# Performance work log

Measured on AMD Instinct MI355X. Metric: run time of the kernel, lower is better.

## Reference

```python
import jax, jax.numpy as jnp
import numpy as np

B, N, D, H = 64, 196, 768, 3072
QMAX = 127.0  # 8-bit symmetric: clamp to [-128, 127]


def ste_round(x):
    # straight-through-estimator round (QAT)
    return x + jax.lax.stop_gradient(jnp.round(x) - x)


def q_linear_diag(x, w, b, a_sf):
    """Quantized diagonal linear (ResMLP Affine / LayerScale as QuantLinear)."""
    w_sf = jnp.max(jnp.abs(w)) / QMAX            # per-tensor weight scale
    w_int = ste_round(w / w_sf)                  # int8 weights (|.|<=127)
    out_int = (x / a_sf) * w_int
    if b is not None:
        out_int = out_int + ste_round(b / (a_sf * w_sf))  # 32-bit bias
    return out_int * (a_sf * w_sf), w_sf


def q_linear_dense(x, w, b, a_sf):
    """Quantized dense linear: int8 GEMM + int32 bias, dequant with a_sf*w_sf."""
    w_sf = jnp.max(jnp.abs(w)) / QMAX
    w_int = jnp.clip(ste_round(w / w_sf), -QMAX - 1, QMAX)
    out_int = jnp.einsum('...i,oi->...o', x / a_sf, w_int) + ste_round(b / (a_sf * w_sf))
    return out_int * (a_sf * w_sf), w_sf


def q_act(x, pre_sf, new_sf, identity=None, id_sf=None):
    """HAWQ-style QuantAct: fixed-point requantization to scale new_sf (8-bit)."""
    if identity is None:
        z_int = ste_round(x / pre_sf)
        out_int = ste_round(z_int * (pre_sf / new_sf))
    else:
        # main branch (x - identity) requantized with pre_sf, identity with id_sf
        z_int = ste_round((x - identity) / pre_sf)
        out_int = ste_round(z_int * (pre_sf / new_sf)) \
                + ste_round(ste_round(identity / id_sf) * (id_sf / new_sf))
    out_int = jnp.clip(out_int, -QMAX - 1, QMAX)
    return out_int * new_sf, new_sf


def _forward(x, norm1_w, norm1_b, attn_w, attn_b, gamma1_w,
             norm2_w, norm2_b, fc1_w, fc1_b, fc2_w, fc2_b, gamma2_w, act_sfs):
    a_sf = act_sfs[0]
    # --- token-mixing half ---
    identity, id_sf = x, a_sf
    x, w_sf = q_linear_diag(x, norm1_w, norm1_b, a_sf)         # norm1 (affine)
    x = jnp.swapaxes(x, 1, 2)                                  # [B, D, N]
    x, a_sf = q_act(x, a_sf * w_sf, act_sfs[1])                # quant_act1
    x, w_sf = q_linear_dense(x, attn_w, attn_b, a_sf)          # attn (cross-patch)
    x = jnp.swapaxes(x, 1, 2)                                  # [B, N, D]
    x, a_sf = q_act(x, a_sf * w_sf, act_sfs[2])                # quant_act2
    x, w_sf = q_linear_diag(x, gamma1_w, None, a_sf)           # gamma_1 (layerscale)
    x = x + identity
    x, a_sf = q_act(x, a_sf * w_sf, act_sfs[3], identity, id_sf)  # quant_act_int32_1
    # --- MLP half ---
    identity, id_sf = x, a_sf
    x, w_sf = q_linear_diag(x, norm2_w, norm2_b, a_sf)         # norm2
    x, a_sf = q_act(x, a_sf * w_sf, act_sfs[4])                # quant_act3
    x, w_sf = q_linear_dense(x, fc1_w, fc1_b, a_sf)            # mlp.fc1
    x = jax.nn.relu(x)
    x, a_sf = q_act(x, a_sf * w_sf, act_sfs[5])                # mlp.quant_act1
    x, w_sf = q_linear_dense(x, fc2_w, fc2_b, a_sf)            # mlp.fc2
    x, a_sf = q_act(x, a_sf * w_sf, act_sfs[6])                # mlp.quant_act2
    x, w_sf = q_linear_diag(x, gamma2_w, None, a_sf)           # gamma_2
    x = x + identity
    x, a_sf = q_act(x, a_sf * w_sf, act_sfs[7], identity, id_sf)  # quant_act_int32_2
    return x, a_sf


def setup_inputs() -> dict:
    key = jax.random.key(0)
    ks = jax.random.split(key, 16)
    act_sfs = jax.random.uniform(ks[14], (8,), jnp.float32, 0.02, 0.06)
    x = jax.random.normal(ks[0], (B, N, D), jnp.float32)
    # input is already quantized at scale act_sfs[0]
    x = jnp.clip(jnp.round(x / act_sfs[0]), -128, 127) * act_sfs[0]
    s = 0.05
    return {
        'x': x,
        'norm1_w': 1.0 + s * jax.random.normal(ks[1], (D,), jnp.float32),
        'norm1_b': s * jax.random.normal(ks[2], (D,), jnp.float32),
        'attn_w': jax.random.normal(ks[3], (N, N), jnp.float32) / np.sqrt(N),
        'attn_b': s * jax.random.normal(ks[4], (N,), jnp.float32),
        'gamma1_w': 0.1 + s * jax.random.normal(ks[5], (D,), jnp.float32),
        'norm2_w': 1.0 + s * jax.random.normal(ks[6], (D,), jnp.float32),
        'norm2_b': s * jax.random.normal(ks[7], (D,), jnp.float32),
        'fc1_w': jax.random.normal(ks[8], (H, D), jnp.float32) / np.sqrt(D),
        'fc1_b': s * jax.random.normal(ks[9], (H,), jnp.float32),
        'fc2_w': jax.random.normal(ks[10], (D, H), jnp.float32) / np.sqrt(H),
        'fc2_b': s * jax.random.normal(ks[11], (D,), jnp.float32),
        'gamma2_w': 0.1 + s * jax.random.normal(ks[12], (D,), jnp.float32),
        'act_sfs': act_sfs,
    }


def reference(x, norm1_w, norm1_b, attn_w, attn_b, gamma1_w,
              norm2_w, norm2_b, fc1_w, fc1_b, fc2_w, fc2_b, gamma2_w, act_sfs):
    return _forward(x, norm1_w, norm1_b, attn_w, attn_b, gamma1_w,
                    norm2_w, norm2_b, fc1_w, fc1_b, fc2_w, fc2_b, gamma2_w, act_sfs)
```

## Files before the change

### kernel.cpp

```cpp
#include <hip/hip_runtime.h>

#define B_ 64
#define N_ 196
#define D_ 768
#define H_ 3072
#define M_ (B_*N_)
#define NP 256

typedef int int4v __attribute__((ext_vector_type(4)));
typedef signed char i8;

#define WS_MAX 0
#define WS_W1F 16
#define WS_B1F (16+768)
#define WS_G1F (16+768*2)
#define WS_W2F (16+768*3)
#define WS_B2F (16+768*4)
#define WS_G2F (16+768*5)
#define WS_BA  (16+768*6)
#define WS_BF1 (WS_BA+256)
#define WS_BF2 (WS_BF1+3072)
#define OFF_WA   40960ull
#define OFF_FC1  (OFF_WA+65536ull)
#define OFF_FC2  (OFF_FC1+2359296ull)
#define OFF_X2   (OFF_FC2+2359296ull)
#define OFF_Q3   (OFF_X2+9633792ull)
#define OFF_Q4   (OFF_Q3+9633792ull)
#define OFF_Q1T  OFF_Q4

__device__ __forceinline__ float clamp8(float v){ return fminf(fmaxf(v,-128.f),127.f); }

__device__ __forceinline__ void async16(const void* g, void* l){
    __builtin_amdgcn_global_load_lds((const __attribute__((address_space(1))) void*)g,
                                     (__attribute__((address_space(3))) void*)l, 16, 0, 0);
}

__global__ void k_init(char* ws, const float* __restrict__ act, float* out_tail){
    int id = blockIdx.x*256 + threadIdx.x;
    if (blockIdx.x == 0){
        float* f = (float*)ws;
        if (threadIdx.x < 8) f[WS_MAX+threadIdx.x] = 0.f;
        if (threadIdx.x == 8) *out_tail = act[7];
    }
    if (id < 4096){ int4v z = {0,0,0,0}; ((int4v*)(ws+OFF_WA))[id] = z; }
}

__global__ void k_maxabs(const float* __restrict__ p0, const float* __restrict__ p1,
                         const float* __restrict__ p2, const float* __restrict__ p3,
                         const float* __restrict__ p4, const float* __restrict__ p5,
                         const float* __restrict__ p6, float* wsmax){
    const float* ps[7] = {p0,p1,p2,p3,p4,p5,p6};
    const int    n4s[7] = {192, 9604, 192, 192, 589824, 589824, 192};
    int tid = blockIdx.y;
    const float4* p = (const float4*)ps[tid]; int n4 = n4s[tid];
    float m = 0.f;
    for (int i = blockIdx.x*blockDim.x + threadIdx.x; i < n4; i += gridDim.x*blockDim.x){
        float4 v = p[i];
        m = fmaxf(m, fmaxf(fmaxf(fabsf(v.x),fabsf(v.y)), fmaxf(fabsf(v.z),fabsf(v.w))));
    }
    #pragma unroll
    for (int off = 32; off; off >>= 1) m = fmaxf(m, __shfl_down(m, off, 64));
    __shared__ float red[4];
    int lane = threadIdx.x & 63, wv = threadIdx.x >> 6;
    if (lane == 0) red[wv] = m;
    __syncthreads();
    if (threadIdx.x == 0){
        float mm = red[0];
        for (int w = 1; w < (int)blockDim.x/64; w++) mm = fmaxf(mm, red[w]);
        atomicMax((unsigned*)&wsmax[tid], __float_as_uint(mm));
    }
}

__global__ void k_qweights(const float* __restrict__ n1w, const float* __restrict__ n1b,
                           const float* __restrict__ aw,  const float* __restrict__ ab,
                           const float* __restrict__ g1w, const float* __restrict__ n2w,
                           const float* __restrict__ n2b, const float* __restrict__ f1w,
                           const float* __restrict__ f1b, const float* __restrict__ f2w,
                           const float* __restrict__ f2b, const float* __restrict__ g2w,
                           const float* __restrict__ act, char* ws){
    float* fws = (float*)ws;
    int*   iws = (int*)ws;
    const float* mx = fws + WS_MAX;
    long i = (long)blockIdx.x*blockDim.x + threadIdx.x;
    const long F4 = 589824;
    if (i < F4){ float sf = mx[4]/127.0f;
        float4 v = ((const float4*)f1w)[i];
        char4 o = make_char4(
            (i8)(int)fminf(fmaxf(rintf(v.x/sf),-128.f),127.f),
            (i8)(int)fminf(fmaxf(rintf(v.y/sf),-128.f),127.f),
            (i8)(int)fminf(fmaxf(rintf(v.z/sf),-128.f),127.f),
            (i8)(int)fminf(fmaxf(rintf(v.w/sf),-128.f),127.f));
        ((char4*)(ws+OFF_FC1))[i] = o; return; }
    i -= F4;
    if (i < F4){ float sf = mx[5]/127.0f;
        float4 v = ((const float4*)f2w)[i];
        char4 o = make_char4(
            (i8)(int)fminf(fmaxf(rintf(v.x/sf),-128.f),127.f),
            (i8)(int)fminf(fmaxf(rintf(v.y/sf),-128.f),127.f),
            (i8)(int)fminf(fmaxf(rintf(v.z/sf),-128.f),127.f),
            (i8)(int)fminf(fmaxf(rintf(v.w/sf),-128.f),127.f));
        ((char4*)(ws+OFF_FC2))[i] = o; return; }
    i -= F4;
    if (i < 38416){ float sf = mx[1]/127.0f;
        int o = (int)(i/196), k = (int)(i%196);
        ((i8*)(ws+OFF_WA))[o*NP+k] = (i8)(int)fminf(fmaxf(rintf(aw[i]/sf),-128.f),127.f); return; }
    i -= 38416;
    if (i < 768){ float sf = mx[0]/127.0f; fws[WS_W1F+i] = rintf(n1w[i]/sf); return; }
    i -= 768;
    if (i < 768){ float sf = mx[0]/127.0f; fws[WS_B1F+i] = rintf(n1b[i]/(act[0]*sf)); return; }
    i -= 768;
    if (i < 768){ float sf = mx[2]/127.0f; fws[WS_G1F+i] = rintf(g1w[i]/sf); return; }
    i -= 768;
    if (i < 768){ float sf = mx[3]/127.0f; fws[WS_W2F+i] = rintf(n2w[i]/sf); return; }
    i -= 768;
    if (i < 768){ float sf = mx[3]/127.0f; fws[WS_B2F+i] = rintf(n2b[i]/(act[3]*sf)); return; }
    i -= 768;
    if (i < 768){ float sf = mx[6]/127.0f; fws[WS_G2F+i] = rintf(g2w[i]/sf); return; }
    i -= 768;
    if (i < 196){ float sf = mx[1]/127.0f; iws[WS_BA+i] = (int)rintf(ab[i]/(act[1]*sf)); return; }
    i -= 196;
    if (i < 3072){ float sf = mx[4]/127.0f; iws[WS_BF1+i] = (int)rintf(f1b[i]/(act[4]*sf)); return; }
    i -= 3072;
    if (i < 768){ float sf = mx[5]/127.0f; iws[WS_BF2+i] = (int)rintf(f2b[i]/(act[5]*sf)); return; }
}

__global__ __launch_bounds__(256) void k_stage1(const float* __restrict__ x,
                                                const char* __restrict__ wsc,
                                                char* __restrict__ ws,
                                                const float* __restrict__ act){
    __shared__ i8 T[64][68];
    const float* fws = (const float*)wsc;
    int b = blockIdx.z, n0 = blockIdx.y*64, d0 = blockIdx.x*64;
    int t = threadIdx.x;
    float a0 = act[0];
    float w1sf = fws[WS_MAX+0]/127.0f;
    float r1 = (a0*w1sf)/act[1];
    int dl = (t & 15) * 4;
    int d  = d0 + dl;
    float4 wv = *(const float4*)(fws + WS_W1F + d);
    float4 bv = *(const float4*)(fws + WS_B1F + d);
    #pragma unroll
    for (int pass = 0; pass < 4; pass++){
        int nl = (t >> 4) + pass*16;
        int n  = n0 + nl;
        i8 q[4] = {0,0,0,0};
        if (n < 196){
            float4 xv = *(const float4*)(x + ((size_t)b*196 + n)*768 + d);
            float o0 = rintf(xv.x/a0*wv.x + bv.x);
            float o1 = rintf(xv.y/a0*wv.y + bv.y);
            float o2 = rintf(xv.z/a0*wv.z + bv.z);
            float o3 = rintf(xv.w/a0*wv.w + bv.w);
            q[0] = (i8)(int)clamp8(rintf(o0*r1));
            q[1] = (i8)(int)clamp8(rintf(o1*r1));
            q[2] = (i8)(int)clamp8(rintf(o2*r1));
            q[3] = (i8)(int)clamp8(rintf(o3*r1));
        }
        T[dl+0][nl] = q[0]; T[dl+1][nl] = q[1];
        T[dl+2][nl] = q[2]; T[dl+3][nl] = q[3];
    }
    __syncthreads();
    i8* q1T = (i8*)(ws + OFF_Q1T) + (size_t)b*768*NP;
    #pragma unroll
    for (int e = 0; e < 4; e++){
        int id = t + e*256;
        int row = id >> 4, c = (id & 15) * 4;
        int v = *(const int*)&T[row][c];
        *(int*)(q1T + (size_t)(d0+row)*NP + n0 + c) = v;
    }
}

__device__ __forceinline__ void gemm_i8_loop(const i8* __restrict__ qa, const i8* __restrict__ wb,
                                             size_t lda, size_t ldb,
                                             int m0, int n0, int K, int4v acc[4][4],
                                             i8* As, i8* Bs, int t){
    int lane = t & 63;
    int w = t >> 6;
    int wm = w & 1, wn = w >> 1;
    int lr = lane >> 2, lc = lane & 3;
    const i8* ga = qa + (size_t)(m0 + w*32 + lr)*lda + lc*16;
    const i8* gb = wb + (size_t)(n0 + w*32 + lr)*ldb + lc*16;
    i8* lA = As + (w*32 + lr)*64 + lc*16;
    i8* lB = Bs + (w*32 + lr)*64 + lc*16;
    for (int kb = 0; kb < K; kb += 64){
        __syncthreads();
        async16(ga + kb,            lA);
        async16(ga + kb + 16*lda,   lA + 16*64);
        async16(gb + kb,            lB);
        async16(gb + kb + 16*ldb,   lB + 16*64);
        __syncthreads();
        int4v a[4], bb[4];
        #pragma unroll
        for (int mt = 0; mt < 4; mt++)
            a[mt] = *(const int4v*)(As + (wm*64+mt*16+(lane&15))*64 + (lane>>4)*16);
        #pragma unroll
        for (int nt = 0; nt < 4; nt++)
            bb[nt] = *(const int4v*)(Bs + (wn*64+nt*16+(lane&15))*64 + (lane>>4)*16);
        #pragma unroll
        for (int mt = 0; mt < 4; mt++)
            #pragma unroll
            for (int nt = 0; nt < 4; nt++)
                acc[mt][nt] = __builtin_amdgcn_mfma_i32_16x16x64_i8(a[mt], bb[nt], acc[mt][nt], 0,0,0);
    }
}

__global__ __launch_bounds__(256) void k_attn(const char* __restrict__ ws,
                                              const float* __restrict__ x,
                                              const float* __restrict__ act){
    __shared__ char smem[32768];
    const float* fws = (const float*)ws;
    const int*   iws = (const int*)ws;
    const i8* A  = (const i8*)(ws + OFF_WA);
    const i8* Bq = (const i8*)(ws + OFF_Q1T) + (size_t)blockIdx.z*768*NP;
    i8* x2 = (i8*)(ws + OFF_X2);
    i8* q3 = (i8*)(ws + OFF_Q3);
    int b = blockIdx.z;
    int m0 = blockIdx.x*128, n0 = blockIdx.y*128;
    int t = threadIdx.x, lane = t & 63;
    int wm = (t>>6)&1, wn = t>>7;
    int4v acc[4][4]; int4v zz = {0,0,0,0};
    #pragma unroll
    for (int mt=0;mt<4;mt++) for (int nt=0;nt<4;nt++) acc[mt][nt] = zz;
    gemm_i8_loop(A, Bq, NP, NP, m0, n0, NP, acc, (i8*)smem, (i8*)smem+8192, t);

    float a0=act[0], a1=act[1], a2=act[2], a3=act[3], a4=act[4];
    float wasf = fws[WS_MAX+1]/127.0f; float r2  = (a1*wasf)/a2;
    float g1sf = fws[WS_MAX+2]/127.0f; float r3a = (a2*g1sf)/a3; float r3b = a0/a3;
    float w2sf = fws[WS_MAX+3]/127.0f; float r4  = (a3*w2sf)/a4;
    float g1v[4], w2v[4], b2v[4];
    #pragma unroll
    for (int nt=0;nt<4;nt++){
        int d = n0 + wn*64 + nt*16 + (lane&15);
        g1v[nt] = fws[WS_G1F + d]; w2v[nt] = fws[WS_W2F + d]; b2v[nt] = fws[WS_B2F + d];
    }
    __syncthreads();
    i8* Xs = (i8*)smem;
    i8* Qs = (i8*)smem + 16384;
    #pragma unroll
    for (int mt=0;mt<4;mt++){
        #pragma unroll
        for (int r=0;r<4;r++){
            int ml = wm*64 + mt*16 + (lane>>4)*4 + r;
            int o  = m0 + ml;
            int ba = iws[WS_BA + o];
            #pragma unroll
            for (int nt=0;nt<4;nt++){
                int nl = wn*64 + nt*16 + (lane&15);
                int d  = n0 + nl;
                float s2 = (float)(acc[mt][nt][r] + ba);
                float q2 = clamp8(rintf(s2*r2));
                float o3v = q2*g1v[nt];
                float xv = (o < 196) ? x[((size_t)b*196 + o)*768 + d] : 0.f;
                float idi = rintf(xv/a0);
                float tt = rintf(o3v*r3a) + rintf(idi*r3b);
                tt = clamp8(tt);
                float o4 = tt*w2v[nt] + b2v[nt];
                float qr = clamp8(rintf(o4*r4));
                Xs[ml*128 + nl] = (i8)(int)tt;
                Qs[ml*128 + nl] = (i8)(int)qr;
            }
        }
    }
    __syncthreads();
    #pragma unroll
    for (int e=0;e<4;e++){
        int id = t + e*256;
        int row = id>>3, c = id&7;
        int o = m0 + row;
        if (o < 196){
            size_t g = ((size_t)b*196 + o)*768 + n0 + c*16;
            *(int4v*)(x2 + g) = *(const int4v*)(Xs + row*128 + c*16);
            *(int4v*)(q3 + g) = *(const int4v*)(Qs + row*128 + c*16);
        }
    }
}

__global__ __launch_bounds__(256) void k_fc1(const char* __restrict__ ws, const float* __restrict__ act){
    __shared__ char smem[16384];
    const float* fws = (const float*)ws;
    const int*   iws = (const int*)ws;
    const i8* qa = (const i8*)(ws+OFF_Q3);
    const i8* wb = (const i8*)(ws+OFF_FC1);
    const int* bias = iws + WS_BF1;
    i8* qout = (i8*)(ws+OFF_Q4);
    int m0 = blockIdx.x*128, n0 = blockIdx.y*128;
    int t = threadIdx.x, lane = t & 63;
    int wm = (t>>6)&1, wn = t>>7;
    int4v acc[4][4]; int4v zz = {0,0,0,0};
    #pragma unroll
    for (int mt=0;mt<4;mt++) for (int nt=0;nt<4;nt++) acc[mt][nt] = zz;
    gemm_i8_loop(qa, wb, 768, 768, m0, n0, 768, acc, (i8*)smem, (i8*)smem+8192, t);
    float wsf = fws[WS_MAX+4]/127.0f;
    float r5 = (act[4]*wsf)/act[5];
    int bcol[4];
    #pragma unroll
    for (int nt=0;nt<4;nt++) bcol[nt] = bias[n0 + wn*64 + nt*16 + (lane&15)];
    __syncthreads();
    i8* Cs = (i8*)smem;
    #pragma unroll
    for (int mt=0;mt<4;mt++){
        #pragma unroll
        for (int nt=0;nt<4;nt++){
            int nl = wn*64 + nt*16 + (lane&15);
            #pragma unroll
            for (int r=0;r<4;r++){
                int s = acc[mt][nt][r] + bcol[nt];
                if (s < 0) s = 0;
                float q = clamp8(rintf((float)s * r5));
                int ml = wm*64 + mt*16 + (lane>>4)*4 + r;
                Cs[ml*128 + nl] = (i8)(int)q;
            }
        }
    }
    __syncthreads();
    #pragma unroll
    for (int e=0;e<4;e++){
        int id2 = t + e*256;
        int row = id2>>3, c = id2&7;
        *(int4v*)(qout + (size_t)(m0+row)*3072 + n0 + c*16) = *(const int4v*)(Cs + row*128 + c*16);
    }
}

__global__ __launch_bounds__(256) void k_fc2(const char* __restrict__ ws, const float* __restrict__ act,
                                             float* __restrict__ out){
    __shared__ char smem[16384];
    const float* fws = (const float*)ws;
    const int*   iws = (const int*)ws;
    const i8* qa = (const i8*)(ws+OFF_Q4);
    const i8* wb = (const i8*)(ws+OFF_FC2);
    const int* bias = iws + WS_BF2;
    const float* g2f = fws + WS_G2F;
    const i8* x2 = (const i8*)(ws+OFF_X2);
    int m0 = blockIdx.x*128, n0 = blockIdx.y*128;
    int t = threadIdx.x, lane = t & 63;
    int wm = (t>>6)&1, wn = t>>7;
    int4v acc[4][4]; int4v zz = {0,0,0,0};
    #pragma unroll
    for (int mt=0;mt<4;mt++) for (int nt=0;nt<4;nt++) acc[mt][nt] = zz;
    gemm_i8_loop(qa, wb, 3072, 3072, m0, n0, 3072, acc, (i8*)smem, (i8*)smem+8192, t);
    float a3=act[3], a5=act[5], a6=act[6], a7=act[7];
    float wsf  = fws[WS_MAX+5]/127.0f; float r6  = (a5*wsf)/a6;
    float g2sf = fws[WS_MAX+6]/127.0f; float r7a = (a6*g2sf)/a7; float r7b = a3/a7;
    int bcol[4]; float g2v[4];
    #pragma unroll
    for (int nt=0;nt<4;nt++){
        int nc = n0 + wn*64 + nt*16 + (lane&15);
        bcol[nt] = bias[nc]; g2v[nt] = g2f[nc];
    }
    #pragma unroll
    for (int mt=0;mt<4;mt++){
        #pragma unroll
        for (int nt=0;nt<4;nt++){
            int nc = n0 + wn*64 + nt*16 + (lane&15);
            #pragma unroll
            for (int r=0;r<4;r++){
                int ml = wm*64 + mt*16 + (lane>>4)*4 + r;
                size_t gi = (size_t)(m0+ml)*768 + nc;
                int s = acc[mt][nt][r] + bcol[nt];
                float q6 = clamp8(rintf((float)s*r6));
                float o7 = q6*g2v[nt];
                float idi = (float)x2[gi];
                float tt = rintf(o7*r7a) + rintf(idi*r7b);
                tt = clamp8(tt);
                out[gi] = tt*a7;
            }
        }
    }
}

extern "C" void kernel_launch(void* const* d_in, const int* in_sizes, int n_in,
                              void* d_out, int out_size, void* d_ws, size_t ws_size,
                              hipStream_t stream){
    const float* x   = (const float*)d_in[0];
    const float* n1w = (const float*)d_in[1];
    const float* n1b = (const float*)d_in[2];
    const float* aw  = (const float*)d_in[3];
    const float* ab  = (const float*)d_in[4];
    const float* g1w = (const float*)d_in[5];
    const float* n2w = (const float*)d_in[6];
    const float* n2b = (const float*)d_in[7];
    const float* f1w = (const float*)d_in[8];
    const float* f1b = (const float*)d_in[9];
    const float* f2w = (const float*)d_in[10];
    const float* f2b = (const float*)d_in[11];
    const float* g2w = (const float*)d_in[12];
    const float* act = (const float*)d_in[13];
    char* ws = (char*)d_ws;
    float* out = (float*)d_out;

    k_init<<<16,256,0,stream>>>(ws, act, out + (size_t)B_*N_*D_);
    k_maxabs<<<dim3(120,7),256,0,stream>>>(n1w, aw, g1w, n2w, f1w, f2w, g2w, (float*)ws);
    long qwThreads = 2L*589824 + 38416 + 768L*6 + 196 + 3072 + 768;
    k_qweights<<<(int)((qwThreads+255)/256),256,0,stream>>>(n1w,n1b,aw,ab,g1w,n2w,n2b,
                                                            f1w,f1b,f2w,f2b,g2w,act,ws);
    k_stage1<<<dim3(12,4,64),256,0,stream>>>(x, ws, ws, act);
    k_attn<<<dim3(2,6,64),256,0,stream>>>(ws, x, act);
    k_fc1<<<dim3(98,24),256,0,stream>>>(ws, act);
    k_fc2<<<dim3(98,6),256,0,stream>>>(ws, act, out);
}
```

Baseline: 303.5 us.

## Load GEMM fragments directly from global memory with register double buffering

Replaces the LDS-staged int8 GEMM main loop (async global-to-LDS copies plus two barriers per k-step) with each wave loading its MFMA A/B fragments straight from global memory into registers. Two register sets are ping-ponged so the next k-slice loads while the current one is multiplied, and the now-unneeded barriers and the fc2 shared buffer are removed. The trade-off is that the two waves sharing a tile row or column each fetch the same data, so cache traffic doubles, the 16-byte loads at large strides are poorly coalesced, and register pressure rises.

```diff
diff --git a/kernel.cpp b/kernel.cpp
--- a/kernel.cpp
+++ b/kernel.cpp
@@ -29,11 +29,6 @@
 #define OFF_Q1T  OFF_Q4
 
 __device__ __forceinline__ float clamp8(float v){ return fminf(fmaxf(v,-128.f),127.f); }
-
-__device__ __forceinline__ void async16(const void* g, void* l){
-    __builtin_amdgcn_global_load_lds((const __attribute__((address_space(1))) void*)g,
-                                     (__attribute__((address_space(3))) void*)l, 16, 0, 0);
-}
 
 __global__ void k_init(char* ws, const float* __restrict__ act, float* out_tail){
     int id = blockIdx.x*256 + threadIdx.x;
@@ -169,37 +164,58 @@
     }
 }
 
-__device__ __forceinline__ void gemm_i8_loop(const i8* __restrict__ qa, const i8* __restrict__ wb,
-                                             size_t lda, size_t ldb,
-                                             int m0, int n0, int K, int4v acc[4][4],
-                                             i8* As, i8* Bs, int t){
+__device__ __forceinline__ void gemm_i8_direct(const i8* __restrict__ qa, const i8* __restrict__ wb,
+                                               size_t lda, size_t ldb,
+                                               int m0, int n0, int K, int4v acc[4][4], int t){
     int lane = t & 63;
-    int w = t >> 6;
-    int wm = w & 1, wn = w >> 1;
-    int lr = lane >> 2, lc = lane & 3;
-    const i8* ga = qa + (size_t)(m0 + w*32 + lr)*lda + lc*16;
-    const i8* gb = wb + (size_t)(n0 + w*32 + lr)*ldb + lc*16;
-    i8* lA = As + (w*32 + lr)*64 + lc*16;
-    i8* lB = Bs + (w*32 + lr)*64 + lc*16;
-    for (int kb = 0; kb < K; kb += 64){
-        __syncthreads();
-        async16(ga + kb,            lA);
-        async16(ga + kb + 16*lda,   lA + 16*64);
-        async16(gb + kb,            lB);
-        async16(gb + kb + 16*ldb,   lB + 16*64);
-        __syncthreads();
-        int4v a[4], bb[4];
-        #pragma unroll
-        for (int mt = 0; mt < 4; mt++)
-            a[mt] = *(const int4v*)(As + (wm*64+mt*16+(lane&15))*64 + (lane>>4)*16);
-        #pragma unroll
-        for (int nt = 0; nt < 4; nt++)
-            bb[nt] = *(const int4v*)(Bs + (wn*64+nt*16+(lane&15))*64 + (lane>>4)*16);
-        #pragma unroll
-        for (int mt = 0; mt < 4; mt++)
-            #pragma unroll
-            for (int nt = 0; nt < 4; nt++)
-                acc[mt][nt] = __builtin_amdgcn_mfma_i32_16x16x64_i8(a[mt], bb[nt], acc[mt][nt], 0,0,0);
+    int wm = (t>>6)&1, wn = t>>7;
+    int fr = lane & 15;
+    int kc = (lane >> 4) * 16;
+    const i8* pa = qa + (size_t)(m0 + wm*64 + fr)*lda + kc;
+    const i8* pb = wb + (size_t)(n0 + wn*64 + fr)*ldb + kc;
+    int4v a0[4], b0[4], a1[4], b1[4];
+    #pragma unroll
+    for (int mt=0;mt<4;mt++) a0[mt] = *(const int4v*)(pa + (size_t)mt*16*lda);
+    #pragma unroll
+    for (int nt=0;nt<4;nt++) b0[nt] = *(const int4v*)(pb + (size_t)nt*16*ldb);
+    int iters = K >> 6;
+    for (int i = 0; i < iters-2; i += 2){
+        int k1 = (i+1) << 6, k2 = (i+2) << 6;
+        #pragma unroll
+        for (int mt=0;mt<4;mt++) a1[mt] = *(const int4v*)(pa + k1 + (size_t)mt*16*lda);
+        #pragma unroll
+        for (int nt=0;nt<4;nt++) b1[nt] = *(const int4v*)(pb + k1 + (size_t)nt*16*ldb);
+        #pragma unroll
+        for (int mt=0;mt<4;mt++)
+            #pragma unroll
+            for (int nt=0;nt<4;nt++)
+                acc[mt][nt] = __builtin_amdgcn_mfma_i32_16x16x64_i8(a0[mt], b0[nt], acc[mt][nt],0,0,0);
+        #pragma unroll
+        for (int mt=0;mt<4;mt++) a0[mt] = *(const int4v*)(pa + k2 + (size_t)mt*16*lda);
+        #pragma unroll
+        for (int nt=0;nt<4;nt++) b0[nt] = *(const int4v*)(pb + k2 + (size_t)nt*16*ldb);
+        #pragma unroll
+        for (int mt=0;mt<4;mt++)
+            #pragma unroll
+            for (int nt=0;nt<4;nt++)
+                acc[mt][nt] = __builtin_amdgcn_mfma_i32_16x16x64_i8(a1[mt], b1[nt], acc[mt][nt],0,0,0);
+    }
+    {
+        int k1 = (iters-1) << 6;
+        #pragma unroll
+        for (int mt=0;mt<4;mt++) a1[mt] = *(const int4v*)(pa + k1 + (size_t)mt*16*lda);
+        #pragma unroll
+        for (int nt=0;nt<4;nt++) b1[nt] = *(const int4v*)(pb + k1 + (size_t)nt*16*ldb);
+        #pragma unroll
+        for (int mt=0;mt<4;mt++)
+            #pragma unroll
+            for (int nt=0;nt<4;nt++)
+                acc[mt][nt] = __builtin_amdgcn_mfma_i32_16x16x64_i8(a0[mt], b0[nt], acc[mt][nt],0,0,0);
+        #pragma unroll
+        for (int mt=0;mt<4;mt++)
+            #pragma unroll
+            for (int nt=0;nt<4;nt++)
+                acc[mt][nt] = __builtin_amdgcn_mfma_i32_16x16x64_i8(a1[mt], b1[nt], acc[mt][nt],0,0,0);
     }
 }
 
@@ -220,7 +236,7 @@
     int4v acc[4][4]; int4v zz = {0,0,0,0};
     #pragma unroll
     for (int mt=0;mt<4;mt++) for (int nt=0;nt<4;nt++) acc[mt][nt] = zz;
-    gemm_i8_loop(A, Bq, NP, NP, m0, n0, NP, acc, (i8*)smem, (i8*)smem+8192, t);
+    gemm_i8_direct(A, Bq, NP, NP, m0, n0, NP, acc, t);
 
     float a0=act[0], a1=act[1], a2=act[2], a3=act[3], a4=act[4];
     float wasf = fws[WS_MAX+1]/127.0f; float r2  = (a1*wasf)/a2;
@@ -232,7 +248,6 @@
         int d = n0 + wn*64 + nt*16 + (lane&15);
         g1v[nt] = fws[WS_G1F + d]; w2v[nt] = fws[WS_W2F + d]; b2v[nt] = fws[WS_B2F + d];
     }
-    __syncthreads();
     i8* Xs = (i8*)smem;
     i8* Qs = (i8*)smem + 16384;
     #pragma unroll
@@ -288,13 +303,12 @@
     int4v acc[4][4]; int4v zz = {0,0,0,0};
     #pragma unroll
     for (int mt=0;mt<4;mt++) for (int nt=0;nt<4;nt++) acc[mt][nt] = zz;
-    gemm_i8_loop(qa, wb, 768, 768, m0, n0, 768, acc, (i8*)smem, (i8*)smem+8192, t);
+    gemm_i8_direct(qa, wb, 768, 768, m0, n0, 768, acc, t);
     float wsf = fws[WS_MAX+4]/127.0f;
     float r5 = (act[4]*wsf)/act[5];
     int bcol[4];
     #pragma unroll
     for (int nt=0;nt<4;nt++) bcol[nt] = bias[n0 + wn*64 + nt*16 + (lane&15)];
-    __syncthreads();
     i8* Cs = (i8*)smem;
     #pragma unroll
     for (int mt=0;mt<4;mt++){
@@ -322,7 +336,6 @@
 
 __global__ __launch_bounds__(256) void k_fc2(const char* __restrict__ ws, const float* __restrict__ act,
                                              float* __restrict__ out){
-    __shared__ char smem[16384];
     const float* fws = (const float*)ws;
     const int*   iws = (const int*)ws;
     const i8* qa = (const i8*)(ws+OFF_Q4);
@@ -336,7 +349,7 @@
     int4v acc[4][4]; int4v zz = {0,0,0,0};
     #pragma unroll
     for (int mt=0;mt<4;mt++) for (int nt=0;nt<4;nt++) acc[mt][nt] = zz;
-    gemm_i8_loop(qa, wb, 3072, 3072, m0, n0, 3072, acc, (i8*)smem, (i8*)smem+8192, t);
+    gemm_i8_direct(qa, wb, 3072, 3072, m0, n0, 3072, acc, t);
     float a3=act[3], a5=act[5], a6=act[6], a7=act[7];
     float wsf  = fws[WS_MAX+5]/127.0f; float r6  = (a5*wsf)/a6;
     float g2sf = fws[WS_MAX+6]/127.0f; float r7a = (a6*g2sf)/a7; float r7b = a3/a7;
```

Measured after the change: 442.8 us. +45.9%, slower.

## Double-buffer LDS tiles in the int8 GEMM loop to overlap loads with MFMA

Applied to the files above, without the earlier changes.

The shared int8 GEMM main loop now uses two LDS buffers per operand. The next K-tile's async global-to-LDS copies are issued before the MFMAs on the current tile, which also removes one of the two barriers per iteration. The aim is to hide global load latency behind compute in the attn, fc1 and fc2 kernels. In exchange, LDS use per block for fc1 and fc2 doubles to 32 KB, which could reduce occupancy.

```diff
diff --git a/kernel.cpp b/kernel.cpp
--- a/kernel.cpp
+++ b/kernel.cpp
@@ -169,7 +169,7 @@
     }
 }
 
-__device__ __forceinline__ void gemm_i8_loop(const i8* __restrict__ qa, const i8* __restrict__ wb,
+__device__ __forceinline__ void gemm_i8_dbuf(const i8* __restrict__ qa, const i8* __restrict__ wb,
                                              size_t lda, size_t ldb,
                                              int m0, int n0, int K, int4v acc[4][4],
                                              i8* As, i8* Bs, int t){
@@ -179,22 +179,30 @@
     int lr = lane >> 2, lc = lane & 3;
     const i8* ga = qa + (size_t)(m0 + w*32 + lr)*lda + lc*16;
     const i8* gb = wb + (size_t)(n0 + w*32 + lr)*ldb + lc*16;
-    i8* lA = As + (w*32 + lr)*64 + lc*16;
-    i8* lB = Bs + (w*32 + lr)*64 + lc*16;
-    for (int kb = 0; kb < K; kb += 64){
+    int loff = (w*32 + lr)*64 + lc*16;
+    async16(ga,            As + loff);
+    async16(ga + 16*lda,   As + loff + 16*64);
+    async16(gb,            Bs + loff);
+    async16(gb + 16*ldb,   Bs + loff + 16*64);
+    int iters = K >> 6;
+    for (int i = 0; i < iters; i++){
         __syncthreads();
-        async16(ga + kb,            lA);
-        async16(ga + kb + 16*lda,   lA + 16*64);
-        async16(gb + kb,            lB);
-        async16(gb + kb + 16*ldb,   lB + 16*64);
-        __syncthreads();
+        if (i+1 < iters){
+            int kb = (i+1) << 6;
+            int nb = ((i+1)&1) << 13;
+            async16(ga + kb,            As + nb + loff);
+            async16(ga + kb + 16*lda,   As + nb + loff + 16*64);
+            async16(gb + kb,            Bs + nb + loff);
+            async16(gb + kb + 16*ldb,   Bs + nb + loff + 16*64);
+        }
+        int cb = (i&1) << 13;
         int4v a[4], bb[4];
         #pragma unroll
         for (int mt = 0; mt < 4; mt++)
-            a[mt] = *(const int4v*)(As + (wm*64+mt*16+(lane&15))*64 + (lane>>4)*16);
+            a[mt] = *(const int4v*)(As + cb + (wm*64+mt*16+(lane&15))*64 + (lane>>4)*16);
         #pragma unroll
         for (int nt = 0; nt < 4; nt++)
-            bb[nt] = *(const int4v*)(Bs + (wn*64+nt*16+(lane&15))*64 + (lane>>4)*16);
+            bb[nt] = *(const int4v*)(Bs + cb + (wn*64+nt*16+(lane&15))*64 + (lane>>4)*16);
         #pragma unroll
         for (int mt = 0; mt < 4; mt++)
             #pragma unroll
@@ -220,7 +228,7 @@
     int4v acc[4][4]; int4v zz = {0,0,0,0};
     #pragma unroll
     for (int mt=0;mt<4;mt++) for (int nt=0;nt<4;nt++) acc[mt][nt] = zz;
-    gemm_i8_loop(A, Bq, NP, NP, m0, n0, NP, acc, (i8*)smem, (i8*)smem+8192, t);
+    gemm_i8_dbuf(A, Bq, NP, NP, m0, n0, NP, acc, (i8*)smem, (i8*)smem+16384, t);
 
     float a0=act[0], a1=act[1], a2=act[2], a3=act[3], a4=act[4];
     float wasf = fws[WS_MAX+1]/127.0f; float r2  = (a1*wasf)/a2;
@@ -275,7 +283,7 @@
 }
 
 __global__ __launch_bounds__(256) void k_fc1(const char* __restrict__ ws, const float* __restrict__ act){
-    __shared__ char smem[16384];
+    __shared__ char smem[32768];
     const float* fws = (const float*)ws;
     const int*   iws = (const int*)ws;
     const i8* qa = (const i8*)(ws+OFF_Q3);
@@ -288,7 +296,7 @@
     int4v acc[4][4]; int4v zz = {0,0,0,0};
     #pragma unroll
     for (int mt=0;mt<4;mt++) for (int nt=0;nt<4;nt++) acc[mt][nt] = zz;
-    gemm_i8_loop(qa, wb, 768, 768, m0, n0, 768, acc, (i8*)smem, (i8*)smem+8192, t);
+    gemm_i8_dbuf(qa, wb, 768, 768, m0, n0, 768, acc, (i8*)smem, (i8*)smem+16384, t);
     float wsf = fws[WS_MAX+4]/127.0f;
     float r5 = (act[4]*wsf)/act[5];
     int bcol[4];
@@ -322,7 +330,7 @@
 
 __global__ __launch_bounds__(256) void k_fc2(const char* __restrict__ ws, const float* __restrict__ act,
                                              float* __restrict__ out){
-    __shared__ char smem[16384];
+    __shared__ char smem[32768];
     const float* fws = (const float*)ws;
     const int*   iws = (const int*)ws;
     const i8* qa = (const i8*)(ws+OFF_Q4);
@@ -336,7 +344,7 @@
     int4v acc[4][4]; int4v zz = {0,0,0,0};
     #pragma unroll
     for (int mt=0;mt<4;mt++) for (int nt=0;nt<4;nt++) acc[mt][nt] = zz;
-    gemm_i8_loop(qa, wb, 3072, 3072, m0, n0, 3072, acc, (i8*)smem, (i8*)smem+8192, t);
+    gemm_i8_dbuf(qa, wb, 3072, 3072, m0, n0, 3072, acc, (i8*)smem, (i8*)smem+16384, t);
     float a3=act[3], a5=act[5], a6=act[6], a7=act[7];
     float wsf  = fws[WS_MAX+5]/127.0f; float r6  = (a5*wsf)/a6;
     float g2sf = fws[WS_MAX+6]/127.0f; float r7a = (a6*g2sf)/a7; float r7b = a3/a7;
```

Result: faster. 280.9 us (-7.4%).
